# Optimization experiments

Hardware: AMD Instinct MI355X
Metric: run time of the kernel (lower is better)

Reference implementation:

```python
import jax, jax.numpy as jnp
import numpy as np

HEADS = 12
EMBED = 768
HEAD_DIM = EMBED // HEADS
SCALING = HEAD_DIM ** (-0.5)


def setup_inputs() -> dict:
    key = jax.random.key(0)
    k1, k2, k3, k4, k5 = jax.random.split(key, 5)
    B, N = 8, 1024
    x = jax.random.normal(k1, (B, N, EMBED), dtype=jnp.float32)
    W_qkv = jax.random.normal(k2, (3 * EMBED, EMBED), dtype=jnp.float32) * 0.02
    b_qkv = jax.random.normal(k3, (3 * EMBED,), dtype=jnp.float32) * 0.02
    W_proj = jax.random.normal(k4, (EMBED, EMBED), dtype=jnp.float32) * 0.02
    b_proj = jax.random.normal(k5, (EMBED,), dtype=jnp.float32) * 0.02
    return {"x": x, "W_qkv": W_qkv, "b_qkv": b_qkv, "W_proj": W_proj, "b_proj": b_proj}


def reference(x, W_qkv, b_qkv, W_proj, b_proj):
    B, N, D = x.shape
    # fused QKV projection: [B, N, 3D]
    qkv = x @ W_qkv.T + b_qkv
    # split last dim as (u=3, h, e) per einops 'b n (u h e) -> u b h n e'
    qkv = qkv.reshape(B, N, 3, HEADS, HEAD_DIM).transpose(2, 0, 3, 1, 4)
    q, k, v = qkv[0], qkv[1], qkv[2]
    # raw dot-product scores (NO pre-softmax scaling, per original)
    sim = jnp.einsum('bhqi,bhki->bhqk', q, k)
    # unusual POST-softmax scaling
    sim = jax.nn.softmax(sim, axis=-1) * SCALING
    att = jnp.einsum('bhnk,bhke->bhne', sim, v)
    att = att.transpose(0, 2, 1, 3).reshape(B, N, D)  # b h n e -> b n (h e)
    return att @ W_proj.T + b_proj
```

## Files before the change

### kernel.cpp

```cpp
#include <hip/hip_runtime.h>

typedef unsigned short u16;
typedef __attribute__((ext_vector_type(8))) short bf16x8;
typedef __attribute__((ext_vector_type(4))) float f32x4;

#define HEADS 12
#define HDIM  64
#define EMBED 768
#define TD    2304
#define SEQ   1024
#define MTOK  8192
#define GK    768
#define GNT   12

__device__ __forceinline__ u16 f2bf(float f) {
  union { float f; unsigned u; } x; x.f = f;
  unsigned r = x.u + 0x7fffu + ((x.u >> 16) & 1u);
  return (u16)(r >> 16);
}

__global__ void cast3_kernel(const float* __restrict__ x, const float* __restrict__ wq,
                             const float* __restrict__ wp, u16* __restrict__ xb,
                             u16* __restrict__ wqb, u16* __restrict__ wpb) {
  const int N1 = MTOK * EMBED / 4, N2 = TD * EMBED / 4, N3 = EMBED * EMBED / 4;
  int i = blockIdx.x * blockDim.x + threadIdx.x;
  int st = gridDim.x * blockDim.x;
  for (; i < N1 + N2 + N3; i += st) {
    const float* s; u16* d; int j;
    if (i < N1)           { s = x;  d = xb;  j = i; }
    else if (i < N1 + N2) { s = wq; d = wqb; j = i - N1; }
    else                  { s = wp; d = wpb; j = i - N1 - N2; }
    float4 v = reinterpret_cast<const float4*>(s)[j];
    ushort4 o;
    o.x = f2bf(v.x); o.y = f2bf(v.y); o.z = f2bf(v.z); o.w = f2bf(v.w);
    reinterpret_cast<ushort4*>(d)[j] = o;
  }
}

__device__ __forceinline__ void gload_lds16(const u16* g, u16* l) {
  __builtin_amdgcn_global_load_lds(
      (const __attribute__((address_space(1))) unsigned*)g,
      (__attribute__((address_space(3))) unsigned*)l, 16, 0, 0);
}

__device__ __forceinline__ void memfence_bar() {
  asm volatile("" ::: "memory");
  __builtin_amdgcn_s_barrier();
  asm volatile("" ::: "memory");
}

template <bool OUT_BF16>
__global__ __launch_bounds__(256, 2) void gemm_min2(const u16* __restrict__ A,
                                                    const u16* __restrict__ B,
                                                    const float* __restrict__ bias,
                                                    void* __restrict__ Cv,
                                                    int NBN, int Ndim) {
  __shared__ u16 As[3][128 * 64];
  __shared__ u16 Bs[2][96 * 64];
  const int tid  = threadIdx.x;
  const int wave = tid >> 6, lane = tid & 63;
  const int wr = wave >> 1, wc = wave & 1;
  const int lr = lane & 15, g = lane >> 4;

  const int nwg = gridDim.x;
  const int swz = (blockIdx.x & 7) * (nwg >> 3) + (blockIdx.x >> 3);
  const int ny = swz % NBN, mx = swz / NBN;

  const u16* Ag = A + (size_t)(mx * 128) * GK;
  const u16* Bg = B + (size_t)(ny * 96) * GK;

  const int srow   = lane >> 3;
  const int schunk = (lane & 7) ^ srow;

  auto stageA = [&](int kt) {
    u16* dst = As[kt % 3];
#pragma unroll
    for (int c = 0; c < 4; ++c) {
      int slot = wave * 4 + c;
      int row  = slot * 8 + srow;
      gload_lds16(Ag + (size_t)row * GK + kt * 64 + schunk * 8, &dst[slot * 512]);
    }
  };
  auto stageB = [&](int kt) {
    u16* dst = Bs[kt & 1];
#pragma unroll
    for (int c = 0; c < 3; ++c) {
      int slot = wave * 3 + c;
      int row  = slot * 8 + srow;
      gload_lds16(Bg + (size_t)row * GK + kt * 64 + schunk * 8, &dst[slot * 512]);
    }
  };

  f32x4 acc[4][3];
#pragma unroll
  for (int m = 0; m < 4; ++m)
#pragma unroll
    for (int n = 0; n < 3; ++n) acc[m][n] = 0.f;

  stageA(0);
  stageB(0);
  stageA(1);
  asm volatile("s_waitcnt vmcnt(4)" ::: "memory");
  memfence_bar();

  for (int t = 0; t < GNT; ++t) {
    if (t + 1 < GNT) stageB(t + 1);
    if (t + 2 < GNT) stageA(t + 2);

    const u16* Ab = As[t % 3];
    const u16* Bb = Bs[t & 1];
    bf16x8 af[4][2], bfr[3][2];
#pragma unroll
    for (int m = 0; m < 4; ++m)
#pragma unroll
      for (int kk = 0; kk < 2; ++kk) {
        int r = wr * 64 + m * 16 + lr;
        af[m][kk] = *reinterpret_cast<const bf16x8*>(
            &Ab[r * 64 + (((kk * 4 + g) ^ (r & 7)) << 3)]);
      }
#pragma unroll
    for (int n = 0; n < 3; ++n)
#pragma unroll
      for (int kk = 0; kk < 2; ++kk) {
        int r = wc * 48 + n * 16 + lr;
        bfr[n][kk] = *reinterpret_cast<const bf16x8*>(
            &Bb[r * 64 + (((kk * 4 + g) ^ (r & 7)) << 3)]);
      }

    __builtin_amdgcn_s_setprio(1);
#pragma unroll
    for (int m = 0; m < 4; ++m)
#pragma unroll
      for (int n = 0; n < 3; ++n) {
        acc[m][n] = __builtin_amdgcn_mfma_f32_16x16x32_bf16(bfr[n][0], af[m][0], acc[m][n], 0, 0, 0);
        acc[m][n] = __builtin_amdgcn_mfma_f32_16x16x32_bf16(bfr[n][1], af[m][1], acc[m][n], 0, 0, 0);
      }
    __builtin_amdgcn_s_setprio(0);

    if (t + 3 <= GNT) {
      asm volatile("s_waitcnt vmcnt(4)" ::: "memory");
      memfence_bar();
    } else if (t + 2 == GNT) {
      asm volatile("s_waitcnt vmcnt(0)" ::: "memory");
      memfence_bar();
    }
  }

  const int row0 = mx * 128 + wr * 64 + lr;
  const int col0 = ny * 96 + wc * 48 + g * 4;
#pragma unroll
  for (int m = 0; m < 4; ++m)
#pragma unroll
    for (int n = 0; n < 3; ++n) {
      int row = row0 + m * 16;
      int col = col0 + n * 16;
      float4 bv = *reinterpret_cast<const float4*>(&bias[col]);
      float v0 = acc[m][n][0] + bv.x, v1 = acc[m][n][1] + bv.y;
      float v2 = acc[m][n][2] + bv.z, v3 = acc[m][n][3] + bv.w;
      if (OUT_BF16) {
        ushort4 pw;
        pw.x = f2bf(v0); pw.y = f2bf(v1); pw.z = f2bf(v2); pw.w = f2bf(v3);
        *reinterpret_cast<ushort4*>(&((u16*)Cv)[(size_t)row * Ndim + col]) = pw;
      } else {
        *reinterpret_cast<float4*>(&((float*)Cv)[(size_t)row * Ndim + col]) =
            make_float4(v0, v1, v2, v3);
      }
    }
}

__global__ __launch_bounds__(256) void vtrans_kernel(const u16* __restrict__ qkv,
                                                     u16* __restrict__ vt) {
  const int bh = blockIdx.x, kb = blockIdx.y;
  const int b = bh / HEADS, h = bh % HEADS;
  __shared__ u16 Ls[64 * 72];
  const int t = threadIdx.x;
  const int row = t >> 2, seg = t & 3;
  const u16* src = qkv + (size_t)(b * SEQ + kb * 64 + row) * TD + 2 * EMBED + h * HDIM + seg * 16;
  *reinterpret_cast<uint4*>(&Ls[row * 72 + seg * 16])     = *reinterpret_cast<const uint4*>(src);
  *reinterpret_cast<uint4*>(&Ls[row * 72 + seg * 16 + 8]) = *reinterpret_cast<const uint4*>(src + 8);
  __syncthreads();
  u16 tmp[16];
#pragma unroll
  for (int i = 0; i < 16; ++i) tmp[i] = Ls[(seg * 16 + i) * 72 + row];
  u16* dst = vt + (size_t)bh * (HDIM * SEQ) + (size_t)row * SEQ + kb * 64 + seg * 16;
  *reinterpret_cast<uint4*>(dst)     = *reinterpret_cast<const uint4*>(tmp);
  *reinterpret_cast<uint4*>(dst + 8) = *reinterpret_cast<const uint4*>(tmp + 8);
}

__global__ __launch_bounds__(256, 3) void attn_kernel(const u16* __restrict__ qkv,
                                                      const u16* __restrict__ vt,
                                                      u16* __restrict__ ctx) {
  const int bh = blockIdx.x;
  const int b = bh / HEADS, h = bh % HEADS;
  const int qt = blockIdx.y;
  const int tid = threadIdx.x, wave = tid >> 6, lane = tid & 63;
  const int lr = lane & 15, g = lane >> 4;

  __shared__ u16 Ks[2][64 * 64];
  __shared__ u16 Vs[2][64 * 64];
  __shared__ u16 Ps[128 * 64];

  const size_t tok0 = (size_t)b * SEQ;
  const int q0 = qt * 128;
  const int mbase = wave * 32;

  bf16x8 qf[2][2];
#pragma unroll
  for (int mi = 0; mi < 2; ++mi)
#pragma unroll
    for (int dk = 0; dk < 2; ++dk)
      qf[mi][dk] = *reinterpret_cast<const bf16x8*>(
          qkv + (tok0 + q0 + mbase + mi * 16 + lr) * TD + h * HDIM + dk * 32 + g * 8);

  const int srow = lane >> 3;
  const int schunk = (lane & 7) ^ srow;
  const u16* vbase = vt + (size_t)bh * (HDIM * SEQ);

  auto stage = [&](int kb, int buf) {
#pragma unroll
    for (int c2 = 0; c2 < 2; ++c2) {
      int call = wave * 2 + c2;
      int row  = call * 8 + srow;
      gload_lds16(qkv + (tok0 + kb * 64 + row) * TD + EMBED + h * HDIM + schunk * 8,
                  &Ks[buf][call * 512]);
      gload_lds16(vbase + (size_t)row * SEQ + kb * 64 + schunk * 8,
                  &Vs[buf][call * 512]);
    }
  };

  f32x4 oacc[2][4];
#pragma unroll
  for (int mi = 0; mi < 2; ++mi)
#pragma unroll
    for (int e = 0; e < 4; ++e) oacc[mi][e] = 0.f;
  float psum[2] = {0.f, 0.f};

  stage(0, 0);
  asm volatile("s_waitcnt vmcnt(0)" ::: "memory");
  memfence_bar();

  int cur = 0;
  for (int kb = 0; kb < 16; ++kb) {
    if (kb < 15) stage(kb + 1, cur ^ 1);

    bf16x8 ka[4][2], vb2[4][2];
#pragma unroll
    for (int n = 0; n < 4; ++n)
#pragma unroll
      for (int dk = 0; dk < 2; ++dk) {
        int r = n * 16 + lr;
        int c = dk * 4 + g;
        ka[n][dk]  = *reinterpret_cast<const bf16x8*>(&Ks[cur][r * 64 + ((c ^ (r & 7)) << 3)]);
        vb2[n][dk] = *reinterpret_cast<const bf16x8*>(&Vs[cur][r * 64 + ((c ^ (r & 7)) << 3)]);
      }

#pragma unroll
    for (int mi = 0; mi < 2; ++mi) {
      int m = mbase + mi * 16 + lr;
      int pswz = (lr & 7) << 1;
#pragma unroll
      for (int n = 0; n < 4; ++n) {
        f32x4 s = 0.f;
        __builtin_amdgcn_s_setprio(1);
        s = __builtin_amdgcn_mfma_f32_16x16x32_bf16(ka[n][0], qf[mi][0], s, 0, 0, 0);
        s = __builtin_amdgcn_mfma_f32_16x16x32_bf16(ka[n][1], qf[mi][1], s, 0, 0, 0);
        __builtin_amdgcn_s_setprio(0);
        float e0 = __expf(s[0]), e1 = __expf(s[1]);
        float e2 = __expf(s[2]), e3 = __expf(s[3]);
        psum[mi] += (e0 + e1) + (e2 + e3);
        ushort4 pw;
        pw.x = f2bf(e0); pw.y = f2bf(e1); pw.z = f2bf(e2); pw.w = f2bf(e3);
        int gran = n * 4 + g;
        *reinterpret_cast<ushort4*>(&Ps[m * 64 + ((gran ^ pswz) << 2)]) = pw;
      }
    }

#pragma unroll
    for (int mi = 0; mi < 2; ++mi) {
      bf16x8 pa[2];
#pragma unroll
      for (int kk = 0; kk < 2; ++kk) {
        int r = mbase + mi * 16 + lr;
        int c = kk * 4 + g;
        pa[kk] = *reinterpret_cast<const bf16x8*>(&Ps[r * 64 + ((c ^ (r & 7)) << 3)]);
      }
      __builtin_amdgcn_s_setprio(1);
#pragma unroll
      for (int e = 0; e < 4; ++e) {
        oacc[mi][e] = __builtin_amdgcn_mfma_f32_16x16x32_bf16(pa[0], vb2[e][0], oacc[mi][e], 0, 0, 0);
        oacc[mi][e] = __builtin_amdgcn_mfma_f32_16x16x32_bf16(pa[1], vb2[e][1], oacc[mi][e], 0, 0, 0);
      }
      __builtin_amdgcn_s_setprio(0);
    }

    if (kb < 15) {
      asm volatile("s_waitcnt vmcnt(0)" ::: "memory");
      memfence_bar();
    }
    cur ^= 1;
  }

  float scl[2][4];
#pragma unroll
  for (int mi = 0; mi < 2; ++mi) {
    float v = psum[mi];
    v += __shfl_xor(v, 16);
    v += __shfl_xor(v, 32);
    v = 0.125f / v;
#pragma unroll
    for (int j = 0; j < 4; ++j) scl[mi][j] = __shfl(v, 4 * g + j);
  }
#pragma unroll
  for (int mi = 0; mi < 2; ++mi)
#pragma unroll
    for (int e = 0; e < 4; ++e)
#pragma unroll
      for (int j = 0; j < 4; ++j) {
        float v = oacc[mi][e][j] * scl[mi][j];
        ctx[(tok0 + q0 + mbase + mi * 16 + 4 * g + j) * EMBED + h * HDIM + e * 16 + lr] = f2bf(v);
      }
}

extern "C" void kernel_launch(void* const* d_in, const int* in_sizes, int n_in,
                              void* d_out, int out_size, void* d_ws, size_t ws_size,
                              hipStream_t stream) {
  (void)in_sizes; (void)n_in; (void)out_size;
  const float* x     = (const float*)d_in[0];
  const float* Wqkv  = (const float*)d_in[1];
  const float* bqkv  = (const float*)d_in[2];
  const float* Wproj = (const float*)d_in[3];
  const float* bproj = (const float*)d_in[4];
  float* out = (float*)d_out;

  char* ws = (char*)d_ws;
  size_t off = 0;
  auto alloc = [&](size_t bytes) {
    char* p = ws + off;
    off += (bytes + 255) & ~(size_t)255;
    return p;
  };
  u16* xb     = (u16*)alloc((size_t)MTOK * EMBED * 2);
  u16* wqkvb  = (u16*)alloc((size_t)TD * EMBED * 2);
  u16* wprojb = (u16*)alloc((size_t)EMBED * EMBED * 2);
  u16* qkvb   = (u16*)alloc((size_t)MTOK * TD * 2);
  u16* ctxb   = (u16*)alloc((size_t)MTOK * EMBED * 2);
  if (off > ws_size) return;
  u16* vtb = xb;

  cast3_kernel<<<dim3(2048), dim3(256), 0, stream>>>(x, Wqkv, Wproj, xb, wqkvb, wprojb);

  gemm_min2<true><<<dim3(1536), dim3(256), 0, stream>>>(xb, wqkvb, bqkv, qkvb, 24, TD);
  vtrans_kernel<<<dim3(96, 16), dim3(256), 0, stream>>>(qkvb, vtb);
  attn_kernel<<<dim3(96, 8), dim3(256), 0, stream>>>(qkvb, vtb, ctxb);
  gemm_min2<false><<<dim3(512), dim3(256), 0, stream>>>(ctxb, wprojb, bproj, out, 8, EMBED);
}
```

Baseline: 125.0 us.

## Add 8-wave 256x128 tiled GEMM kernel for QKV projection

Replaces the 128x96 tile, 4-wave QKV projection GEMM with a new 512-thread kernel that computes 256x128 output tiles. It uses double-buffered direct-to-LDS loads staged in chunks interleaved with two MFMA half-phases per K step, and raises wave priority around the MFMA bursts. Larger tiles give more operand reuse per LDS byte and fewer global reloads. In exchange there is one workgroup per CU, 576 workgroups over 256 CUs (2.25 waves, so tail imbalance), and heavier register use.

```diff
diff --git a/kernel.cpp b/kernel.cpp
--- a/kernel.cpp
+++ b/kernel.cpp
@@ -49,6 +49,117 @@
   asm volatile("" ::: "memory");
 }
 
+__global__ __launch_bounds__(512, 1) void gemm8(const u16* __restrict__ A,
+                                                const u16* __restrict__ B,
+                                                const float* __restrict__ bias,
+                                                u16* __restrict__ Cv,
+                                                int NBN, int Ndim) {
+  __shared__ u16 As[2][256 * 64];
+  __shared__ u16 Bs[2][128 * 64];
+  const int tid  = threadIdx.x;
+  const int wave = tid >> 6, lane = tid & 63;
+  const int wr = wave >> 2, wc = wave & 3;
+  const int lr = lane & 15, g = lane >> 4;
+
+  const int nwg = gridDim.x;
+  const int swz = (blockIdx.x & 7) * (nwg >> 3) + (blockIdx.x >> 3);
+  const int ny = swz % NBN, mx = swz / NBN;
+
+  const u16* Ag = A + (size_t)(mx * 256) * GK;
+  const u16* Bg = B + (size_t)(ny * 128) * GK;
+
+  const int crow = wave * 8 + (lane >> 3);
+  const int ccol = (lane & 7) ^ (crow & 7);
+
+  auto stageAc = [&](int kt, int c) {
+    gload_lds16(Ag + (size_t)(c * 64 + crow) * GK + kt * 64 + ccol * 8,
+                &As[kt & 1][c * 4096 + wave * 512]);
+  };
+  auto stageBc = [&](int kt, int c) {
+    gload_lds16(Bg + (size_t)(c * 64 + crow) * GK + kt * 64 + ccol * 8,
+                &Bs[kt & 1][c * 4096 + wave * 512]);
+  };
+
+  f32x4 acc[8][2];
+#pragma unroll
+  for (int m = 0; m < 8; ++m)
+#pragma unroll
+    for (int n = 0; n < 2; ++n) acc[m][n] = 0.f;
+
+  auto phase = [&](const u16* Ab, const u16* Bb, int aro, f32x4 (*accq)[2],
+                   auto stagefn) {
+    bf16x8 af[4][2], bf[2][2];
+#pragma unroll
+    for (int i = 0; i < 4; ++i) {
+      int r = wr * 128 + aro + i * 16 + lr;
+#pragma unroll
+      for (int ks = 0; ks < 2; ++ks)
+        af[i][ks] = *reinterpret_cast<const bf16x8*>(
+            &Ab[r * 64 + (((ks * 4 + g) ^ (r & 7)) << 3)]);
+    }
+#pragma unroll
+    for (int j = 0; j < 2; ++j) {
+      int r = wc * 32 + j * 16 + lr;
+#pragma unroll
+      for (int ks = 0; ks < 2; ++ks)
+        bf[j][ks] = *reinterpret_cast<const bf16x8*>(
+            &Bb[r * 64 + (((ks * 4 + g) ^ (r & 7)) << 3)]);
+    }
+    stagefn();
+    memfence_bar();
+    asm volatile("s_waitcnt lgkmcnt(0)" ::: "memory");
+    __builtin_amdgcn_sched_barrier(0);
+    __builtin_amdgcn_s_setprio(1);
+#pragma unroll
+    for (int i = 0; i < 4; ++i)
+#pragma unroll
+      for (int j = 0; j < 2; ++j) {
+        accq[i][j] = __builtin_amdgcn_mfma_f32_16x16x32_bf16(bf[j][0], af[i][0], accq[i][j], 0, 0, 0);
+        accq[i][j] = __builtin_amdgcn_mfma_f32_16x16x32_bf16(bf[j][1], af[i][1], accq[i][j], 0, 0, 0);
+      }
+    __builtin_amdgcn_s_setprio(0);
+  };
+
+  stageAc(0, 0); stageAc(0, 1); stageAc(0, 2); stageAc(0, 3);
+  stageBc(0, 0); stageBc(0, 1);
+  stageAc(1, 0); stageAc(1, 2);
+  asm volatile("s_waitcnt vmcnt(2)" ::: "memory");
+  memfence_bar();
+
+  for (int t = 0; t < GNT; ++t) {
+    const u16* Ab = As[t & 1];
+    const u16* Bb = Bs[t & 1];
+    phase(Ab, Bb, 0, &acc[0], [&] {
+      if (t + 1 < GNT) { stageAc(t + 1, 1); stageAc(t + 1, 3); stageBc(t + 1, 0); }
+    });
+    memfence_bar();
+    phase(Ab, Bb, 64, &acc[4], [&] {
+      if (t + 1 < GNT) stageBc(t + 1, 1);
+      if (t + 2 < GNT) { stageAc(t + 2, 0); stageAc(t + 2, 2); }
+    });
+    if (t + 2 < GNT)      { asm volatile("s_waitcnt vmcnt(2)" ::: "memory"); }
+    else if (t + 1 < GNT) { asm volatile("s_waitcnt vmcnt(0)" ::: "memory"); }
+    memfence_bar();
+  }
+
+  const int row0 = mx * 256 + wr * 128 + lr;
+  const int col0 = ny * 128 + wc * 32 + g * 4;
+#pragma unroll
+  for (int m = 0; m < 8; ++m)
+#pragma unroll
+    for (int n = 0; n < 2; ++n) {
+      int row = row0 + m * 16;
+      int col = col0 + n * 16;
+      float4 bv = *reinterpret_cast<const float4*>(&bias[col]);
+      ushort4 pw;
+      pw.x = f2bf(acc[m][n][0] + bv.x);
+      pw.y = f2bf(acc[m][n][1] + bv.y);
+      pw.z = f2bf(acc[m][n][2] + bv.z);
+      pw.w = f2bf(acc[m][n][3] + bv.w);
+      *reinterpret_cast<ushort4*>(&Cv[(size_t)row * Ndim + col]) = pw;
+    }
+}
+
 template <bool OUT_BF16>
 __global__ __launch_bounds__(256, 2) void gemm_min2(const u16* __restrict__ A,
                                                     const u16* __restrict__ B,
@@ -349,7 +460,7 @@
 
   cast3_kernel<<<dim3(2048), dim3(256), 0, stream>>>(x, Wqkv, Wproj, xb, wqkvb, wprojb);
 
-  gemm_min2<true><<<dim3(1536), dim3(256), 0, stream>>>(xb, wqkvb, bqkv, qkvb, 24, TD);
+  gemm8<<<dim3(576), dim3(512), 0, stream>>>(xb, wqkvb, bqkv, qkvb, 18, TD);
   vtrans_kernel<<<dim3(96, 16), dim3(256), 0, stream>>>(qkvb, vtb);
   attn_kernel<<<dim3(96, 8), dim3(256), 0, stream>>>(qkvb, vtb, ctxb);
   gemm_min2<false><<<dim3(512), dim3(256), 0, stream>>>(ctxb, wprojb, bproj, out, 8, EMBED);
```

After: 138.3 us. +10.7%, slower.

## Fuse V transpose and log2e scaling into QKV GEMM epilogue

Applied to the files above, without the earlier changes.

Replaces the generic QKV GEMM plus separate V-transpose kernel with a dedicated GEMM. Each workgroup keeps one A row block and walks the Q, K and V column segments, so the A tile is reused across the three segments. The Q output is pre-multiplied by log2(e) so attention can use exp2f instead of __expf, and V is written transposed straight from the epilogue. This removes one kernel launch and a full read and write of V, but the transposed V stores are scattered 2-byte writes, and the grid shrinks from 1536 to 512 longer-running workgroups.

```diff
diff --git a/kernel.cpp b/kernel.cpp
--- a/kernel.cpp
+++ b/kernel.cpp
@@ -12,6 +12,7 @@
 #define MTOK  8192
 #define GK    768
 #define GNT   12
+#define LOG2E 1.4426950408889634f
 
 __device__ __forceinline__ u16 f2bf(float f) {
   union { float f; unsigned u; } x; x.f = f;
@@ -49,6 +50,149 @@
   asm volatile("" ::: "memory");
 }
 
+__global__ __launch_bounds__(256, 2) void gemm_qkv(const u16* __restrict__ A,
+                                                   const u16* __restrict__ B,
+                                                   const float* __restrict__ bias,
+                                                   u16* __restrict__ Cq,
+                                                   u16* __restrict__ vt) {
+  __shared__ u16 As[3][128 * 64];
+  __shared__ u16 Bs[2][96 * 64];
+  const int tid  = threadIdx.x;
+  const int wave = tid >> 6, lane = tid & 63;
+  const int wr = wave >> 1, wc = wave & 1;
+  const int lr = lane & 15, g = lane >> 4;
+
+  const int swz = (blockIdx.x & 7) * 64 + (blockIdx.x >> 3);
+  const int ny = swz & 7, mx = swz >> 3;
+
+  const u16* Ag = A + (size_t)(mx * 128) * GK;
+
+  const int srow   = lane >> 3;
+  const int schunk = (lane & 7) ^ srow;
+
+  auto stageA = [&](int u) {
+    u16* dst = As[u % 3];
+    const int k0 = (u % GNT) * 64;
+#pragma unroll
+    for (int c = 0; c < 4; ++c) {
+      int slot = wave * 4 + c;
+      int row  = slot * 8 + srow;
+      gload_lds16(Ag + (size_t)row * GK + k0 + schunk * 8, &dst[slot * 512]);
+    }
+  };
+  auto stageB = [&](int u) {
+    u16* dst = Bs[u & 1];
+    const int k0 = (u % GNT) * 64;
+    const u16* Bg = B + (size_t)((ny + (u / GNT) * 8) * 96) * GK;
+#pragma unroll
+    for (int c = 0; c < 3; ++c) {
+      int slot = wave * 3 + c;
+      int row  = slot * 8 + srow;
+      gload_lds16(Bg + (size_t)row * GK + k0 + schunk * 8, &dst[slot * 512]);
+    }
+  };
+
+  f32x4 acc[4][3];
+#pragma unroll
+  for (int m = 0; m < 4; ++m)
+#pragma unroll
+    for (int n = 0; n < 3; ++n) acc[m][n] = 0.f;
+
+  const int TOT = 3 * GNT;
+  stageA(0);
+  stageB(0);
+  stageA(1);
+  asm volatile("s_waitcnt vmcnt(4)" ::: "memory");
+  memfence_bar();
+
+  for (int u = 0; u < TOT; ++u) {
+    if (u + 1 < TOT) stageB(u + 1);
+    if (u + 2 < TOT) stageA(u + 2);
+
+    const u16* Ab = As[u % 3];
+    const u16* Bb = Bs[u & 1];
+    bf16x8 af[4][2], bfr[3][2];
+#pragma unroll
+    for (int m = 0; m < 4; ++m)
+#pragma unroll
+      for (int kk = 0; kk < 2; ++kk) {
+        int r = wr * 64 + m * 16 + lr;
+        af[m][kk] = *reinterpret_cast<const bf16x8*>(
+            &Ab[r * 64 + (((kk * 4 + g) ^ (r & 7)) << 3)]);
+      }
+#pragma unroll
+    for (int n = 0; n < 3; ++n)
+#pragma unroll
+      for (int kk = 0; kk < 2; ++kk) {
+        int r = wc * 48 + n * 16 + lr;
+        bfr[n][kk] = *reinterpret_cast<const bf16x8*>(
+            &Bb[r * 64 + (((kk * 4 + g) ^ (r & 7)) << 3)]);
+      }
+
+    __builtin_amdgcn_s_setprio(1);
+#pragma unroll
+    for (int m = 0; m < 4; ++m)
+#pragma unroll
+      for (int n = 0; n < 3; ++n) {
+        acc[m][n] = __builtin_amdgcn_mfma_f32_16x16x32_bf16(bfr[n][0], af[m][0], acc[m][n], 0, 0, 0);
+        acc[m][n] = __builtin_amdgcn_mfma_f32_16x16x32_bf16(bfr[n][1], af[m][1], acc[m][n], 0, 0, 0);
+      }
+    __builtin_amdgcn_s_setprio(0);
+
+    if (u + 3 <= TOT) {
+      asm volatile("s_waitcnt vmcnt(4)" ::: "memory");
+      memfence_bar();
+    } else if (u + 2 == TOT) {
+      asm volatile("s_waitcnt vmcnt(0)" ::: "memory");
+      memfence_bar();
+    }
+
+    if ((u % GNT) == GNT - 1) {
+      const int seg = u / GNT;
+      const int row0 = mx * 128 + wr * 64 + lr;
+      const int colb = (ny + seg * 8) * 96 + wc * 48 + g * 4;
+      if (seg < 2) {
+        const float sc = (seg == 0) ? LOG2E : 1.f;
+#pragma unroll
+        for (int m = 0; m < 4; ++m)
+#pragma unroll
+          for (int n = 0; n < 3; ++n) {
+            int row = row0 + m * 16;
+            int col = colb + n * 16;
+            float4 bv = *reinterpret_cast<const float4*>(&bias[col]);
+            ushort4 pw;
+            pw.x = f2bf((acc[m][n][0] + bv.x) * sc);
+            pw.y = f2bf((acc[m][n][1] + bv.y) * sc);
+            pw.z = f2bf((acc[m][n][2] + bv.z) * sc);
+            pw.w = f2bf((acc[m][n][3] + bv.w) * sc);
+            *reinterpret_cast<ushort4*>(&Cq[(size_t)row * TD + col]) = pw;
+            acc[m][n] = 0.f;
+          }
+      } else {
+#pragma unroll
+        for (int m = 0; m < 4; ++m) {
+          int row = row0 + m * 16;
+          int b   = row >> 10;
+          int tk  = row & 1023;
+#pragma unroll
+          for (int n = 0; n < 3; ++n) {
+            int col = colb + n * 16;
+            float4 bv = *reinterpret_cast<const float4*>(&bias[col]);
+#pragma unroll
+            for (int j = 0; j < 4; ++j) {
+              int vcol = col + j - 2 * EMBED;
+              int h = vcol >> 6, e = vcol & 63;
+              float v = acc[m][n][j] + (j == 0 ? bv.x : j == 1 ? bv.y : j == 2 ? bv.z : bv.w);
+              vt[((size_t)(b * HEADS + h) * HDIM + e) * SEQ + tk] = f2bf(v);
+            }
+            acc[m][n] = 0.f;
+          }
+        }
+      }
+    }
+  }
+}
+
 template <bool OUT_BF16>
 __global__ __launch_bounds__(256, 2) void gemm_min2(const u16* __restrict__ A,
                                                     const u16* __restrict__ B,
@@ -168,25 +312,6 @@
     }
 }
 
-__global__ __launch_bounds__(256) void vtrans_kernel(const u16* __restrict__ qkv,
-                                                     u16* __restrict__ vt) {
-  const int bh = blockIdx.x, kb = blockIdx.y;
-  const int b = bh / HEADS, h = bh % HEADS;
-  __shared__ u16 Ls[64 * 72];
-  const int t = threadIdx.x;
-  const int row = t >> 2, seg = t & 3;
-  const u16* src = qkv + (size_t)(b * SEQ + kb * 64 + row) * TD + 2 * EMBED + h * HDIM + seg * 16;
-  *reinterpret_cast<uint4*>(&Ls[row * 72 + seg * 16])     = *reinterpret_cast<const uint4*>(src);
-  *reinterpret_cast<uint4*>(&Ls[row * 72 + seg * 16 + 8]) = *reinterpret_cast<const uint4*>(src + 8);
-  __syncthreads();
-  u16 tmp[16];
-#pragma unroll
-  for (int i = 0; i < 16; ++i) tmp[i] = Ls[(seg * 16 + i) * 72 + row];
-  u16* dst = vt + (size_t)bh * (HDIM * SEQ) + (size_t)row * SEQ + kb * 64 + seg * 16;
-  *reinterpret_cast<uint4*>(dst)     = *reinterpret_cast<const uint4*>(tmp);
-  *reinterpret_cast<uint4*>(dst + 8) = *reinterpret_cast<const uint4*>(tmp + 8);
-}
-
 __global__ __launch_bounds__(256, 3) void attn_kernel(const u16* __restrict__ qkv,
                                                       const u16* __restrict__ vt,
                                                       u16* __restrict__ ctx) {
@@ -265,8 +390,8 @@
         s = __builtin_amdgcn_mfma_f32_16x16x32_bf16(ka[n][0], qf[mi][0], s, 0, 0, 0);
         s = __builtin_amdgcn_mfma_f32_16x16x32_bf16(ka[n][1], qf[mi][1], s, 0, 0, 0);
         __builtin_amdgcn_s_setprio(0);
-        float e0 = __expf(s[0]), e1 = __expf(s[1]);
-        float e2 = __expf(s[2]), e3 = __expf(s[3]);
+        float e0 = exp2f(s[0]), e1 = exp2f(s[1]);
+        float e2 = exp2f(s[2]), e3 = exp2f(s[3]);
         psum[mi] += (e0 + e1) + (e2 + e3);
         ushort4 pw;
         pw.x = f2bf(e0); pw.y = f2bf(e1); pw.z = f2bf(e2); pw.w = f2bf(e3);
@@ -344,13 +469,12 @@
   u16* wprojb = (u16*)alloc((size_t)EMBED * EMBED * 2);
   u16* qkvb   = (u16*)alloc((size_t)MTOK * TD * 2);
   u16* ctxb   = (u16*)alloc((size_t)MTOK * EMBED * 2);
+  u16* vtb    = (u16*)alloc((size_t)MTOK * EMBED * 2);
   if (off > ws_size) return;
-  u16* vtb = xb;
 
   cast3_kernel<<<dim3(2048), dim3(256), 0, stream>>>(x, Wqkv, Wproj, xb, wqkvb, wprojb);
 
-  gemm_min2<true><<<dim3(1536), dim3(256), 0, stream>>>(xb, wqkvb, bqkv, qkvb, 24, TD);
-  vtrans_kernel<<<dim3(96, 16), dim3(256), 0, stream>>>(qkvb, vtb);
+  gemm_qkv<<<dim3(512), dim3(256), 0, stream>>>(xb, wqkvb, bqkv, qkvb, vtb);
   attn_kernel<<<dim3(96, 8), dim3(256), 0, stream>>>(qkvb, vtb, ctxb);
   gemm_min2<false><<<dim3(512), dim3(256), 0, stream>>>(ctxb, wprojb, bproj, out, 8, EMBED);
 }
```

Result: no change. 125.9 us (+0.7%).
